# Performance work log

Hardware: AMD Instinct MI355X
Metric: run time of the kernel (lower is better)

## Reference

```python
import jax, jax.numpy as jnp
import numpy as np

TEMPERATURE = 0.1
LARGE_NUM = 1e9


def _l2_normalize(x, eps=1e-12):
    # tf.math.l2_normalize: x * rsqrt(max(sum(x^2), eps))
    sq = jnp.sum(x * x, axis=-1, keepdims=True)
    return x * jax.lax.rsqrt(jnp.maximum(sq, eps))


def setup_inputs() -> dict:
    key = jax.random.key(0)
    k1, k2 = jax.random.split(key)
    B, D = 4096, 128
    z1 = jax.random.normal(k1, (B, D), dtype=jnp.float32)
    z2 = jax.random.normal(k2, (B, D), dtype=jnp.float32)
    return {"z1": z1, "z2": z2}


def reference(z1, z2):
    B = z1.shape[0]
    a = _l2_normalize(z1)  # [B, D]
    b = _l2_normalize(z2)  # [B, D]
    mask = jnp.eye(B, dtype=a.dtype)
    inv_t = 1.0 / TEMPERATURE
    logits_aa = jnp.matmul(a, a.T) * inv_t - mask * LARGE_NUM  # [B, B]
    logits_bb = jnp.matmul(b, b.T) * inv_t - mask * LARGE_NUM  # [B, B]
    logits_ab = jnp.matmul(a, b.T) * inv_t                      # [B, B]
    logits_ba = jnp.matmul(b, a.T) * inv_t                      # [B, B]
    part1 = jax.nn.softmax(jnp.concatenate([logits_ab, logits_aa], axis=1), axis=-1)
    part2 = jax.nn.softmax(jnp.concatenate([logits_ba, logits_bb], axis=1), axis=-1)
    return jnp.concatenate([part1, part2], axis=1)  # [B, 4B]
```

## Files before the change

### kernel.cpp

```cpp
#include <hip/hip_runtime.h>
#include <hip/hip_fp16.h>
#include <cstdint>
#include <cstddef>

#define NB   4096
#define ND   128
#define OUTW 16384
#define CG   16
#define IT   (8192 / CG / 64)

#define K2   14.4269504088896341f

typedef _Float16 f16;
typedef __attribute__((ext_vector_type(2))) _Float16 f16x2;
typedef __attribute__((ext_vector_type(8))) _Float16 f16x8;
typedef __attribute__((ext_vector_type(4))) float   f32x4;

__global__ __launch_bounds__(256) void nrm_kernel(const float* __restrict__ z1,
                                                  const float* __restrict__ z2,
                                                  f16* __restrict__ ab,
                                                  float* __restrict__ rowsum) {
  if (threadIdx.x < 4) rowsum[blockIdx.x * 4 + threadIdx.x] = 0.0f;
  int row  = blockIdx.x * 4 + (threadIdx.x >> 6);
  int lane = threadIdx.x & 63;
  const float* src = (row < NB) ? (z1 + (size_t)row * ND)
                                : (z2 + (size_t)(row - NB) * ND);
  float2 v = ((const float2*)src)[lane];
  float ss = v.x * v.x + v.y * v.y;
#pragma unroll
  for (int off = 32; off; off >>= 1) ss += __shfl_xor(ss, off);
  float r = rsqrtf(fmaxf(ss, 1e-12f));
  f16x2 h;
  h.x = (f16)(v.x * r);
  h.y = (f16)(v.y * r);
  ((f16x2*)(ab + (size_t)row * ND))[lane] = h;
}

template <bool WRITE>
__global__ __launch_bounds__(256, 2) void pass_kernel(const f16* __restrict__ ab,
                                                      float* __restrict__ rowsum,
                                                      float* __restrict__ out) {
  __shared__ f16 Bs[2][64 * ND];
  __shared__ float cs[128];

  const int t    = threadIdx.x;
  const int wave = t >> 6;
  const int lane = t & 63;
  const int wr   = wave >> 1;
  const int wc   = wave & 1;
  const int quad = lane >> 4;
  const int l16  = lane & 15;

  const int rt    = blockIdx.y;
  const int type  = rt >> 5;
  const int r0    = (rt & 31) * 128;
  const int g     = blockIdx.x;
  const int h2    = (g >= CG / 2) ? 1 : 0;
  const int cbl   = g * (8192 / CG);
  const int cbase = cbl & (NB - 1);
  const f16* Q  = ab + (size_t)type * NB * ND;
  const f16* Kp = ab + (size_t)(h2 ? type : (type ^ 1)) * NB * ND;

  f16x8 af[4][4];
  {
    const int arow = r0 + wr * 64 + l16;
#pragma unroll
    for (int mi = 0; mi < 4; ++mi)
#pragma unroll
      for (int ks = 0; ks < 4; ++ks)
        af[mi][ks] = *(const f16x8*)(Q + (size_t)(arow + mi * 16) * ND +
                                     ks * 32 + quad * 8);
  }

  const int sub = t >> 4;
  const int oct = t & 15;
  auto stage_b = [&](f16* buf, int kc0) {
#pragma unroll
    for (int i = 0; i < 4; ++i) {
      int rowl = i * 16 + sub;
      int goct = oct ^ (rowl & 15);
      __builtin_amdgcn_global_load_lds(
          (const __attribute__((address_space(1))) void*)(
              Kp + (size_t)(kc0 + rowl) * ND + goct * 8),
          (__attribute__((address_space(3))) void*)(buf + rowl * ND + oct * 8),
          16, 0, 0);
    }
  };

  float ps[4];
  if (!WRITE) {
#pragma unroll
    for (int mi = 0; mi < 4; ++mi) ps[mi] = 0.0f;
  }

  stage_b(Bs[0], cbase);
  if (WRITE) {
    if (t < 128) cs[t] = -__log2f(rowsum[rt * 128 + t]) - K2;
  }
  __syncthreads();

  for (int it = 0; it < IT; ++it) {
    if (it + 1 < IT) stage_b(Bs[(it + 1) & 1], cbase + (it + 1) * 64);

    const f16* buf = Bs[it & 1];
    f32x4 acc[4][2] = {};
#pragma unroll
    for (int ks = 0; ks < 4; ++ks) {
      int sw = (((ks * 4 + quad) ^ l16)) * 8;
      f16x8 bf0 = *(const f16x8*)(buf + (wc * 32 + l16) * ND + sw);
      f16x8 bf1 = *(const f16x8*)(buf + (wc * 32 + 16 + l16) * ND + sw);
#pragma unroll
      for (int mi = 0; mi < 4; ++mi) {
        acc[mi][0] = __builtin_amdgcn_mfma_f32_16x16x32_f16(bf0, af[mi][ks],
                                                            acc[mi][0], 0, 0, 0);
        acc[mi][1] = __builtin_amdgcn_mfma_f32_16x16x32_f16(bf1, af[mi][ks],
                                                            acc[mi][1], 0, 0, 0);
      }
    }

    const int c0m = cbase + it * 64;
    const bool dtile = h2 && (c0m == r0 || c0m == r0 + 64);

    if (WRITE) {
#pragma unroll
      for (int mi = 0; mi < 4; ++mi) {
        const int row_l = wr * 64 + mi * 16 + l16;
        const float c = cs[row_l];
        float* orow = out + (size_t)(r0 + row_l) * OUTW + (size_t)type * 8192 +
                      cbl + it * 64;
#pragma unroll
        for (int ni = 0; ni < 2; ++ni) {
          const int cq = wc * 32 + ni * 16 + quad * 4;
          f32x4 o;
#pragma unroll
          for (int r = 0; r < 4; ++r) {
            float e = __builtin_amdgcn_exp2f(fmaf(acc[mi][ni][r], K2, c));
            if (dtile && (c0m + cq + r == r0 + row_l)) e = 0.0f;
            o[r] = e;
          }
          *(f32x4*)(orow + cq) = o;
        }
      }
    } else {
#pragma unroll
      for (int mi = 0; mi < 4; ++mi) {
        const int row_l = wr * 64 + mi * 16 + l16;
#pragma unroll
        for (int ni = 0; ni < 2; ++ni) {
          const int cq = wc * 32 + ni * 16 + quad * 4;
#pragma unroll
          for (int r = 0; r < 4; ++r) {
            float e = __builtin_amdgcn_exp2f(fmaf(acc[mi][ni][r], K2, -K2));
            if (dtile && (c0m + cq + r == r0 + row_l)) e = 0.0f;
            ps[mi] += e;
          }
        }
      }
    }
    __syncthreads();
  }

  if (!WRITE) {
#pragma unroll
    for (int mi = 0; mi < 4; ++mi) {
      float v = ps[mi];
      v += __shfl_xor(v, 16);
      v += __shfl_xor(v, 32);
      if (quad == 0) {
        int row_l = wr * 64 + mi * 16 + l16;
        atomicAdd(&rowsum[rt * 128 + row_l], v);
      }
    }
  }
}

extern "C" void kernel_launch(void* const* d_in, const int* in_sizes, int n_in,
                              void* d_out, int out_size, void* d_ws, size_t ws_size,
                              hipStream_t stream) {
  const float* z1 = (const float*)d_in[0];
  const float* z2 = (const float*)d_in[1];
  float* out = (float*)d_out;

  f16* ab = (f16*)d_ws;
  float* rowsum = (float*)((char*)d_ws + (size_t)8192 * ND * sizeof(f16));

  nrm_kernel<<<2048, 256, 0, stream>>>(z1, z2, ab, rowsum);
  dim3 grid(CG, 64);
  pass_kernel<false><<<grid, 256, 0, stream>>>(ab, rowsum, out);
  pass_kernel<true><<<grid, 256, 0, stream>>>(ab, rowsum, out);
}
```

Before: 300.6 us.

## Exploit symmetry of a·bᵀ to compute row sums with three matmul blocks instead of four

The row-sum pass now computes only the aa, bb and ab blocks. Column sums of the ab block are accumulated through LDS and atomics to stand in for the row sums of ba, since ba is the transpose of ab. This removes a quarter of the MFMA and exp work in the first pass. In exchange it adds shuffle reductions, shared-memory atomics and extra global atomics. The write pass is unchanged, and IT stays 8 in both kernels.

```diff
diff --git a/kernel.cpp b/kernel.cpp
--- a/kernel.cpp
+++ b/kernel.cpp
@@ -7,7 +7,7 @@
 #define ND   128
 #define OUTW 16384
 #define CG   16
-#define IT   (8192 / CG / 64)
+#define IT   8
 
 #define K2   14.4269504088896341f
 
@@ -36,10 +36,147 @@
   ((f16x2*)(ab + (size_t)row * ND))[lane] = h;
 }
 
-template <bool WRITE>
-__global__ __launch_bounds__(256, 2) void pass_kernel(const f16* __restrict__ ab,
-                                                      float* __restrict__ rowsum,
-                                                      float* __restrict__ out) {
+__global__ __launch_bounds__(256, 2) void sum_kernel(const f16* __restrict__ ab,
+                                                     float* __restrict__ rowsum) {
+  __shared__ f16 Bs[2][64 * ND];
+  __shared__ float cs_col[512];
+
+  const int t    = threadIdx.x;
+  const int wave = t >> 6;
+  const int lane = t & 63;
+  const int wr   = wave >> 1;
+  const int wc   = wave & 1;
+  const int quad = lane >> 4;
+  const int l16  = lane & 15;
+
+  const int s     = blockIdx.y;
+  const int m     = s >> 5;
+  const int r0    = (s & 31) * 128;
+  const int cbase = blockIdx.x * 512;
+  const f16* Q  = ab + (size_t)(m == 2 ? NB * ND : 0);
+  const f16* Kp = ab + (size_t)(m == 1 ? 0 : NB * ND);
+  const bool diag = (m != 0);
+  const bool docol = (m == 0);
+
+  f16x8 af[4][4];
+  {
+    const int arow = r0 + wr * 64 + l16;
+#pragma unroll
+    for (int mi = 0; mi < 4; ++mi)
+#pragma unroll
+      for (int ks = 0; ks < 4; ++ks)
+        af[mi][ks] = *(const f16x8*)(Q + (size_t)(arow + mi * 16) * ND +
+                                     ks * 32 + quad * 8);
+  }
+
+  const int sub = t >> 4;
+  const int oct = t & 15;
+  auto stage_b = [&](f16* buf, int kc0) {
+#pragma unroll
+    for (int i = 0; i < 4; ++i) {
+      int rowl = i * 16 + sub;
+      int goct = oct ^ (rowl & 15);
+      __builtin_amdgcn_global_load_lds(
+          (const __attribute__((address_space(1))) void*)(
+              Kp + (size_t)(kc0 + rowl) * ND + goct * 8),
+          (__attribute__((address_space(3))) void*)(buf + rowl * ND + oct * 8),
+          16, 0, 0);
+    }
+  };
+
+  float ps[4];
+#pragma unroll
+  for (int mi = 0; mi < 4; ++mi) ps[mi] = 0.0f;
+
+  stage_b(Bs[0], cbase);
+  cs_col[t] = 0.0f;
+  cs_col[t + 256] = 0.0f;
+  __syncthreads();
+
+  for (int it = 0; it < IT; ++it) {
+    if (it + 1 < IT) stage_b(Bs[(it + 1) & 1], cbase + (it + 1) * 64);
+
+    const f16* buf = Bs[it & 1];
+    f32x4 acc[4][2] = {};
+#pragma unroll
+    for (int ks = 0; ks < 4; ++ks) {
+      int sw = (((ks * 4 + quad) ^ l16)) * 8;
+      f16x8 bf0 = *(const f16x8*)(buf + (wc * 32 + l16) * ND + sw);
+      f16x8 bf1 = *(const f16x8*)(buf + (wc * 32 + 16 + l16) * ND + sw);
+#pragma unroll
+      for (int mi = 0; mi < 4; ++mi) {
+        acc[mi][0] = __builtin_amdgcn_mfma_f32_16x16x32_f16(bf0, af[mi][ks],
+                                                            acc[mi][0], 0, 0, 0);
+        acc[mi][1] = __builtin_amdgcn_mfma_f32_16x16x32_f16(bf1, af[mi][ks],
+                                                            acc[mi][1], 0, 0, 0);
+      }
+    }
+
+    const int c0m = cbase + it * 64;
+    const bool dtile = diag && (c0m == r0 || c0m == r0 + 64);
+
+    float cpart[8];
+#pragma unroll
+    for (int v = 0; v < 8; ++v) cpart[v] = 0.0f;
+
+#pragma unroll
+    for (int mi = 0; mi < 4; ++mi) {
+      const int row_l = wr * 64 + mi * 16 + l16;
+#pragma unroll
+      for (int ni = 0; ni < 2; ++ni) {
+        const int cq = wc * 32 + ni * 16 + quad * 4;
+#pragma unroll
+        for (int r = 0; r < 4; ++r) {
+          float e = __builtin_amdgcn_exp2f(fmaf(acc[mi][ni][r], K2, -K2));
+          if (dtile && (c0m + cq + r == r0 + row_l)) e = 0.0f;
+          ps[mi] += e;
+          cpart[ni * 4 + r] += e;
+        }
+      }
+    }
+
+    if (docol) {
+#pragma unroll
+      for (int v = 0; v < 8; ++v) {
+        float x = cpart[v];
+        x += __shfl_xor(x, 1);
+        x += __shfl_xor(x, 2);
+        x += __shfl_xor(x, 4);
+        x += __shfl_xor(x, 8);
+        cpart[v] = x;
+      }
+      if (l16 == 0) {
+#pragma unroll
+        for (int v = 0; v < 8; ++v) {
+          int col_l = it * 64 + wc * 32 + (v >> 2) * 16 + quad * 4 + (v & 3);
+          atomicAdd(&cs_col[col_l], cpart[v]);
+        }
+      }
+    }
+    __syncthreads();
+  }
+
+  const int rbase = (m == 2) ? NB + r0 : r0;
+#pragma unroll
+  for (int mi = 0; mi < 4; ++mi) {
+    float v = ps[mi];
+    v += __shfl_xor(v, 16);
+    v += __shfl_xor(v, 32);
+    if (quad == 0) {
+      int row_l = wr * 64 + mi * 16 + l16;
+      atomicAdd(&rowsum[rbase + row_l], v);
+    }
+  }
+
+  if (docol) {
+    atomicAdd(&rowsum[NB + cbase + t], cs_col[t]);
+    atomicAdd(&rowsum[NB + cbase + t + 256], cs_col[t + 256]);
+  }
+}
+
+__global__ __launch_bounds__(256, 2) void wr_kernel(const f16* __restrict__ ab,
+                                                    float* __restrict__ rowsum,
+                                                    float* __restrict__ out) {
   __shared__ f16 Bs[2][64 * ND];
   __shared__ float cs[128];
 
@@ -87,16 +224,8 @@
     }
   };
 
-  float ps[4];
-  if (!WRITE) {
-#pragma unroll
-    for (int mi = 0; mi < 4; ++mi) ps[mi] = 0.0f;
-  }
-
   stage_b(Bs[0], cbase);
-  if (WRITE) {
-    if (t < 128) cs[t] = -__log2f(rowsum[rt * 128 + t]) - K2;
-  }
+  if (t < 128) cs[t] = -__log2f(rowsum[rt * 128 + t]) - K2;
   __syncthreads();
 
   for (int it = 0; it < IT; ++it) {
@@ -121,56 +250,26 @@
     const int c0m = cbase + it * 64;
     const bool dtile = h2 && (c0m == r0 || c0m == r0 + 64);
 
-    if (WRITE) {
-#pragma unroll
-      for (int mi = 0; mi < 4; ++mi) {
-        const int row_l = wr * 64 + mi * 16 + l16;
-        const float c = cs[row_l];
-        float* orow = out + (size_t)(r0 + row_l) * OUTW + (size_t)type * 8192 +
-                      cbl + it * 64;
-#pragma unroll
-        for (int ni = 0; ni < 2; ++ni) {
-          const int cq = wc * 32 + ni * 16 + quad * 4;
-          f32x4 o;
-#pragma unroll
-          for (int r = 0; r < 4; ++r) {
-            float e = __builtin_amdgcn_exp2f(fmaf(acc[mi][ni][r], K2, c));
-            if (dtile && (c0m + cq + r == r0 + row_l)) e = 0.0f;
-            o[r] = e;
-          }
-          *(f32x4*)(orow + cq) = o;
+#pragma unroll
+    for (int mi = 0; mi < 4; ++mi) {
+      const int row_l = wr * 64 + mi * 16 + l16;
+      const float c = cs[row_l];
+      float* orow = out + (size_t)(r0 + row_l) * OUTW + (size_t)type * 8192 +
+                    cbl + it * 64;
+#pragma unroll
+      for (int ni = 0; ni < 2; ++ni) {
+        const int cq = wc * 32 + ni * 16 + quad * 4;
+        f32x4 o;
+#pragma unroll
+        for (int r = 0; r < 4; ++r) {
+          float e = __builtin_amdgcn_exp2f(fmaf(acc[mi][ni][r], K2, c));
+          if (dtile && (c0m + cq + r == r0 + row_l)) e = 0.0f;
+          o[r] = e;
         }
-      }
-    } else {
-#pragma unroll
-      for (int mi = 0; mi < 4; ++mi) {
-        const int row_l = wr * 64 + mi * 16 + l16;
-#pragma unroll
-        for (int ni = 0; ni < 2; ++ni) {
-          const int cq = wc * 32 + ni * 16 + quad * 4;
-#pragma unroll
-          for (int r = 0; r < 4; ++r) {
-            float e = __builtin_amdgcn_exp2f(fmaf(acc[mi][ni][r], K2, -K2));
-            if (dtile && (c0m + cq + r == r0 + row_l)) e = 0.0f;
-            ps[mi] += e;
-          }
-        }
+        *(f32x4*)(orow + cq) = o;
       }
     }
     __syncthreads();
-  }
-
-  if (!WRITE) {
-#pragma unroll
-    for (int mi = 0; mi < 4; ++mi) {
-      float v = ps[mi];
-      v += __shfl_xor(v, 16);
-      v += __shfl_xor(v, 32);
-      if (quad == 0) {
-        int row_l = wr * 64 + mi * 16 + l16;
-        atomicAdd(&rowsum[rt * 128 + row_l], v);
-      }
-    }
   }
 }
 
@@ -185,7 +284,6 @@
   float* rowsum = (float*)((char*)d_ws + (size_t)8192 * ND * sizeof(f16));
 
   nrm_kernel<<<2048, 256, 0, stream>>>(z1, z2, ab, rowsum);
-  dim3 grid(CG, 64);
-  pass_kernel<false><<<grid, 256, 0, stream>>>(ab, rowsum, out);
-  pass_kernel<true><<<grid, 256, 0, stream>>>(ab, rowsum, out);
-}
+  sum_kernel<<<dim3(8, 96), 256, 0, stream>>>(ab, rowsum);
+  wr_kernel<<<dim3(CG, 64), 256, 0, stream>>>(ab, rowsum, out);
+}
```

New measurement: 302.1 us. No clear change (+0.5%).

## Split write pass into strip kernel staging output through LDS with nontemporal stores

Applied to the files above, without the earlier changes.

Replaces the templated write pass with a dedicated kernel. Each block owns a 32-row strip of one half and sweeps all 8192 columns. Results are staged in swizzled shared memory, so each wave can write full 1 KB contiguous row segments with nontemporal stores, aiming for better coalescing and less cache pollution on the 256 MB output. The trade-off is only 256 blocks, more LDS per block, and smaller MFMA tiles per wave with extra barriers, which may reduce occupancy and compute efficiency.

```diff
diff --git a/kernel.cpp b/kernel.cpp
--- a/kernel.cpp
+++ b/kernel.cpp
@@ -7,7 +7,7 @@
 #define ND   128
 #define OUTW 16384
 #define CG   16
-#define IT   (8192 / CG / 64)
+#define IT   8
 
 #define K2   14.4269504088896341f
 
@@ -36,12 +36,9 @@
   ((f16x2*)(ab + (size_t)row * ND))[lane] = h;
 }
 
-template <bool WRITE>
-__global__ __launch_bounds__(256, 2) void pass_kernel(const f16* __restrict__ ab,
-                                                      float* __restrict__ rowsum,
-                                                      float* __restrict__ out) {
+__global__ __launch_bounds__(256, 2) void sum_kernel(const f16* __restrict__ ab,
+                                                     float* __restrict__ rowsum) {
   __shared__ f16 Bs[2][64 * ND];
-  __shared__ float cs[128];
 
   const int t    = threadIdx.x;
   const int wave = t >> 6;
@@ -56,8 +53,7 @@
   const int r0    = (rt & 31) * 128;
   const int g     = blockIdx.x;
   const int h2    = (g >= CG / 2) ? 1 : 0;
-  const int cbl   = g * (8192 / CG);
-  const int cbase = cbl & (NB - 1);
+  const int cbase = (g * 512) & (NB - 1);
   const f16* Q  = ab + (size_t)type * NB * ND;
   const f16* Kp = ab + (size_t)(h2 ? type : (type ^ 1)) * NB * ND;
 
@@ -88,15 +84,10 @@
   };
 
   float ps[4];
-  if (!WRITE) {
-#pragma unroll
-    for (int mi = 0; mi < 4; ++mi) ps[mi] = 0.0f;
-  }
+#pragma unroll
+  for (int mi = 0; mi < 4; ++mi) ps[mi] = 0.0f;
 
   stage_b(Bs[0], cbase);
-  if (WRITE) {
-    if (t < 128) cs[t] = -__log2f(rowsum[rt * 128 + t]) - K2;
-  }
   __syncthreads();
 
   for (int it = 0; it < IT; ++it) {
@@ -121,55 +112,131 @@
     const int c0m = cbase + it * 64;
     const bool dtile = h2 && (c0m == r0 || c0m == r0 + 64);
 
-    if (WRITE) {
-#pragma unroll
-      for (int mi = 0; mi < 4; ++mi) {
-        const int row_l = wr * 64 + mi * 16 + l16;
-        const float c = cs[row_l];
-        float* orow = out + (size_t)(r0 + row_l) * OUTW + (size_t)type * 8192 +
-                      cbl + it * 64;
-#pragma unroll
-        for (int ni = 0; ni < 2; ++ni) {
-          const int cq = wc * 32 + ni * 16 + quad * 4;
-          f32x4 o;
-#pragma unroll
-          for (int r = 0; r < 4; ++r) {
-            float e = __builtin_amdgcn_exp2f(fmaf(acc[mi][ni][r], K2, c));
-            if (dtile && (c0m + cq + r == r0 + row_l)) e = 0.0f;
-            o[r] = e;
-          }
-          *(f32x4*)(orow + cq) = o;
+#pragma unroll
+    for (int mi = 0; mi < 4; ++mi) {
+      const int row_l = wr * 64 + mi * 16 + l16;
+#pragma unroll
+      for (int ni = 0; ni < 2; ++ni) {
+        const int cq = wc * 32 + ni * 16 + quad * 4;
+#pragma unroll
+        for (int r = 0; r < 4; ++r) {
+          float e = __builtin_amdgcn_exp2f(fmaf(acc[mi][ni][r], K2, -K2));
+          if (dtile && (c0m + cq + r == r0 + row_l)) e = 0.0f;
+          ps[mi] += e;
         }
       }
-    } else {
-#pragma unroll
-      for (int mi = 0; mi < 4; ++mi) {
-        const int row_l = wr * 64 + mi * 16 + l16;
-#pragma unroll
-        for (int ni = 0; ni < 2; ++ni) {
-          const int cq = wc * 32 + ni * 16 + quad * 4;
-#pragma unroll
-          for (int r = 0; r < 4; ++r) {
-            float e = __builtin_amdgcn_exp2f(fmaf(acc[mi][ni][r], K2, -K2));
-            if (dtile && (c0m + cq + r == r0 + row_l)) e = 0.0f;
-            ps[mi] += e;
-          }
-        }
-      }
     }
     __syncthreads();
   }
 
-  if (!WRITE) {
-#pragma unroll
-    for (int mi = 0; mi < 4; ++mi) {
-      float v = ps[mi];
-      v += __shfl_xor(v, 16);
-      v += __shfl_xor(v, 32);
-      if (quad == 0) {
-        int row_l = wr * 64 + mi * 16 + l16;
-        atomicAdd(&rowsum[rt * 128 + row_l], v);
-      }
+#pragma unroll
+  for (int mi = 0; mi < 4; ++mi) {
+    float v = ps[mi];
+    v += __shfl_xor(v, 16);
+    v += __shfl_xor(v, 32);
+    if (quad == 0) {
+      int row_l = wr * 64 + mi * 16 + l16;
+      atomicAdd(&rowsum[rt * 128 + row_l], v);
+    }
+  }
+}
+
+__global__ __launch_bounds__(256, 2) void wr_kernel(const f16* __restrict__ ab,
+                                                    float* __restrict__ rowsum,
+                                                    float* __restrict__ out) {
+  __shared__ f16 Bs[2][64 * ND];
+  __shared__ float ob[32 * 256];
+  __shared__ float cs[32];
+
+  const int t    = threadIdx.x;
+  const int w    = t >> 6;
+  const int lane = t & 63;
+  const int quad = lane >> 4;
+  const int l16  = lane & 15;
+  const int sub  = t >> 4;
+  const int oct  = t & 15;
+
+  const int half  = blockIdx.x & 1;
+  const int strip = blockIdx.x >> 1;
+  const int r0    = strip * 32;
+
+  const f16* Q      = ab + (size_t)half * NB * ND;
+  const f16* Kcross = ab + (size_t)(half ^ 1) * NB * ND;
+  const f16* Kown   = Q;
+
+  f16x8 af[2][4];
+#pragma unroll
+  for (int mi = 0; mi < 2; ++mi)
+#pragma unroll
+    for (int ks = 0; ks < 4; ++ks)
+      af[mi][ks] = *(const f16x8*)(Q + (size_t)(r0 + mi * 16 + l16) * ND +
+                                   ks * 32 + quad * 8);
+
+  auto stage_b = [&](f16* buf, int it) {
+    const f16* Kp = (it < 64) ? Kcross : Kown;
+    const int kc0 = (it & 63) * 64;
+#pragma unroll
+    for (int i = 0; i < 4; ++i) {
+      int rowl = i * 16 + sub;
+      int goct = oct ^ (rowl & 15);
+      __builtin_amdgcn_global_load_lds(
+          (const __attribute__((address_space(1))) void*)(
+              Kp + (size_t)(kc0 + rowl) * ND + goct * 8),
+          (__attribute__((address_space(3))) void*)(buf + rowl * ND + oct * 8),
+          16, 0, 0);
+    }
+  };
+
+  stage_b(Bs[0], 0);
+  if (t < 32) cs[t] = -__log2f(rowsum[half * NB + r0 + t]) - K2;
+  __syncthreads();
+
+  for (int it = 0; it < 128; ++it) {
+    if (it + 1 < 128) stage_b(Bs[(it + 1) & 1], it + 1);
+
+    const f16* buf = Bs[it & 1];
+    f32x4 acc[2] = {};
+#pragma unroll
+    for (int ks = 0; ks < 4; ++ks) {
+      int sw = (((ks * 4 + quad) ^ l16)) * 8;
+      f16x8 bf = *(const f16x8*)(buf + (w * 16 + l16) * ND + sw);
+#pragma unroll
+      for (int mi = 0; mi < 2; ++mi)
+        acc[mi] = __builtin_amdgcn_mfma_f32_16x16x32_f16(bf, af[mi][ks],
+                                                         acc[mi], 0, 0, 0);
+    }
+
+    const int cm   = (it - 64) * 64;
+    const bool dtile = (it >= 64) && (cm == (r0 & ~63));
+
+#pragma unroll
+    for (int mi = 0; mi < 2; ++mi) {
+      const int row32 = mi * 16 + l16;
+      const float c = cs[row32];
+      f32x4 o;
+#pragma unroll
+      for (int r = 0; r < 4; ++r) {
+        float e = __builtin_amdgcn_exp2f(fmaf(acc[mi][r], K2, c));
+        if (dtile && (cm + w * 16 + quad * 4 + r == r0 + row32)) e = 0.0f;
+        o[r] = e;
+      }
+      const int c4 = (it & 3) * 16 + w * 4 + quad;
+      const int c4s = c4 ^ (row32 & 7);
+      *(f32x4*)&ob[row32 * 256 + c4s * 4] = o;
+    }
+    __syncthreads();
+
+    if ((it & 3) == 3) {
+      const int fc = (it >> 2) * 256;
+#pragma unroll
+      for (int rr = 0; rr < 8; ++rr) {
+        const int row32 = w * 8 + rr;
+        f32x4 v = *(const f32x4*)&ob[row32 * 256 + (lane ^ (row32 & 7)) * 4];
+        __builtin_nontemporal_store(
+            v, (f32x4*)(out + (size_t)(r0 + row32) * OUTW + half * 8192 + fc +
+                        lane * 4));
+      }
+      __syncthreads();
     }
   }
 }
@@ -185,7 +252,6 @@
   float* rowsum = (float*)((char*)d_ws + (size_t)8192 * ND * sizeof(f16));
 
   nrm_kernel<<<2048, 256, 0, stream>>>(z1, z2, ab, rowsum);
-  dim3 grid(CG, 64);
-  pass_kernel<false><<<grid, 256, 0, stream>>>(ab, rowsum, out);
-  pass_kernel<true><<<grid, 256, 0, stream>>>(ab, rowsum, out);
-}
+  sum_kernel<<<dim3(CG, 64), 256, 0, stream>>>(ab, rowsum);
+  wr_kernel<<<256, 256, 0, stream>>>(ab, rowsum, out);
+}
```

After: 387.2 us. 1.29x slower.
